# Kernel optimization log

Measured on AMD Instinct MI355X. Metric: run time of the kernel, lower is better.

## Reference

```python
import jax, jax.numpy as jnp
import numpy as np

TEMPERATURE = 0.5
BATCH_SIZE = 4096
EPS = 1e-8  # torch.nn.CosineSimilarity default eps


def setup_inputs() -> dict:
    key = jax.random.key(0)
    k1, k2 = jax.random.split(key)
    z1 = jax.random.normal(k1, (BATCH_SIZE, 256), dtype=jnp.float32)
    z2 = jax.random.normal(k2, (BATCH_SIZE, 256), dtype=jnp.float32)
    return {"z1": z1, "z2": z2}


def reference(z1, z2):
    B = z1.shape[0]
    N = 2 * B
    reps = jnp.concatenate([z1, z2], axis=0)  # [N, D]
    # Cosine similarity (torch clamps each norm to eps before dividing)
    norms = jnp.maximum(jnp.linalg.norm(reps, axis=1, keepdims=True), EPS)
    z = reps / norms
    sim = z @ z.T  # [N, N] cosine similarity matrix

    # positives: diagonals at offsets +B and -B (they are identical by symmetry,
    # but keep the original concat order: [diag(+B), diag(-B)])
    l_pos = jnp.diagonal(sim, offset=B)
    r_pos = jnp.diagonal(sim, offset=-B)
    positives = jnp.concatenate([l_pos, r_pos])  # [N]

    inv_t = 1.0 / TEMPERATURE
    pos_logit = positives * inv_t  # logits[:, 0]

    # negatives are all off-diagonal entries of each row (the positive pair is
    # thus present twice in the logits, faithful to the original). CE with
    # label 0 => loss_i = logsumexp(logits_i) - logits_i[0].
    neg_logits = jnp.where(jnp.eye(N, dtype=bool), -jnp.inf, sim * inv_t)
    lse = jnp.logaddexp(pos_logit, jax.scipy.special.logsumexp(neg_logits, axis=1))
    loss = jnp.sum(lse - pos_logit) / N
    return loss
```

## Files before the change

### kernel.cpp

```cpp
#include <hip/hip_runtime.h>
#include <hip/hip_bf16.h>
#include <cstdint>
#include <cstddef>
#include <math.h>

#define BSZ   4096
#define NROW  8192
#define DIM   256
#define INV_T 2.0f
#define EPS_N 1e-8f

typedef __attribute__((ext_vector_type(8))) short bf16x8;
typedef __attribute__((ext_vector_type(4))) float f32x4;

__device__ __forceinline__ unsigned short f2bf(float x) {
    __hip_bfloat16 h = __float2bfloat16(x);
    return __builtin_bit_cast(unsigned short, h);
}

__device__ __forceinline__ void load_lds16(const void* g, void* l) {
    __builtin_amdgcn_global_load_lds(
        (const __attribute__((address_space(1))) void*)g,
        (__attribute__((address_space(3))) void*)l,
        16, 0, 0);
}

__global__ __launch_bounds__(256)
void nt_normalize(const float* __restrict__ z1,
                  const float* __restrict__ z2,
                  char* __restrict__ zn2,
                  float* __restrict__ rowsum) {
    const int wave = threadIdx.x >> 6;
    const int lane = threadIdx.x & 63;
    const int row  = blockIdx.x * 4 + wave;
    const float* src = (row < BSZ) ? (z1 + (size_t)row * DIM)
                                   : (z2 + (size_t)(row - BSZ) * DIM);
    const float4 v = ((const float4*)src)[lane];
    float ss = v.x * v.x + v.y * v.y + v.z * v.z + v.w * v.w;
    #pragma unroll
    for (int off = 32; off; off >>= 1) ss += __shfl_xor(ss, off);
    const float rinv = 1.0f / fmaxf(sqrtf(ss), EPS_N);
    ushort4 o;
    o.x = f2bf(v.x * rinv);
    o.y = f2bf(v.y * rinv);
    o.z = f2bf(v.z * rinv);
    o.w = f2bf(v.w * rinv);
    const int s    = row >> 7;
    const int lrow = row & 127;
    const int kc   = lane >> 4;
    const int unit = (lane >> 1) & 7;
    const int half = lane & 1;
    const int u    = unit ^ (lrow & 7);
    *(ushort4*)(zn2 + (size_t)s * 65536 + kc * 16384 + lrow * 128 + u * 16 + half * 8) = o;
    if (lane == 0) rowsum[row] = 0.0f;
}

__global__ __launch_bounds__(256)
void nt_gram(const char* __restrict__ zn2,
             float* __restrict__ rowsum,
             float* __restrict__ pos) {
    const int l = blockIdx.x;
    int bi = (int)((129.0 - sqrt(16641.0 - 8.0 * (double)l)) * 0.5);
    while (64 * (bi + 1) - (bi + 1) * bi / 2 <= l) ++bi;
    while (64 * bi - bi * (bi - 1) / 2 > l) --bi;
    const int bj = bi + (l - (64 * bi - bi * (bi - 1) / 2));

    __shared__ char As[16384];
    __shared__ char Bs[16384];

    const int t    = threadIdx.x;
    const int lane = t & 63;
    const int wave = t >> 6;
    const int wrow = (wave >> 1) * 64;
    const int wcol = (wave & 1) * 64;
    const int q    = lane >> 4;
    const int r16  = lane & 15;
    const int sw   = r16 & 7;

    const char* A2 = zn2 + (size_t)bi * 65536;
    const char* B2 = zn2 + (size_t)bj * 65536;

    f32x4 acc[4][4] = {};

    for (int kc = 0; kc < 4; ++kc) {
        #pragma unroll
        for (int p = 0; p < 4; ++p)
            load_lds16(A2 + kc * 16384 + p * 4096 + t * 16, As + p * 4096 + t * 16);
        #pragma unroll
        for (int p = 0; p < 4; ++p)
            load_lds16(B2 + kc * 16384 + p * 4096 + t * 16, Bs + p * 4096 + t * 16);
        __syncthreads();

        #pragma unroll
        for (int kk = 0; kk < 64; kk += 32) {
            const int cc   = (kk >> 3) + q;
            const int cpos = (cc ^ sw) << 4;
            bf16x8 af[4], bfr[4];
            #pragma unroll
            for (int mi = 0; mi < 4; ++mi)
                af[mi] = *(const bf16x8*)(As + (wrow + mi * 16 + r16) * 128 + cpos);
            #pragma unroll
            for (int ni = 0; ni < 4; ++ni)
                bfr[ni] = *(const bf16x8*)(Bs + (wcol + ni * 16 + r16) * 128 + cpos);
            #pragma unroll
            for (int mi = 0; mi < 4; ++mi)
                #pragma unroll
                for (int ni = 0; ni < 4; ++ni)
                    acc[mi][ni] = __builtin_amdgcn_mfma_f32_16x16x32_bf16(
                        af[mi], bfr[ni], acc[mi][ni], 0, 0, 0);
        }
        __syncthreads();
    }

    const int c = r16;
    const bool diag_block = (bi == bj);
    float colp[4] = {0.f, 0.f, 0.f, 0.f};

    #pragma unroll
    for (int mi = 0; mi < 4; ++mi) {
        #pragma unroll
        for (int r = 0; r < 4; ++r) {
            const int grow = bi * 128 + wrow + mi * 16 + q * 4 + r;
            float s = 0.f;
            #pragma unroll
            for (int ni = 0; ni < 4; ++ni) {
                const int gcol = bj * 128 + wcol + ni * 16 + c;
                const float val = acc[mi][ni][r];
                float e = __expf(val * INV_T);
                e = (grow == gcol) ? 0.f : e;
                s += e;
                colp[ni] += e;
                if (gcol == grow + BSZ) {
                    pos[grow] = val;
                    pos[gcol] = val;
                }
            }
            s += __shfl_xor(s, 1);
            s += __shfl_xor(s, 2);
            s += __shfl_xor(s, 4);
            s += __shfl_xor(s, 8);
            if (c == 0) atomicAdd(&rowsum[grow], s);
        }
    }
    if (!diag_block) {
        #pragma unroll
        for (int ni = 0; ni < 4; ++ni) {
            float cs = colp[ni];
            cs += __shfl_xor(cs, 16);
            cs += __shfl_xor(cs, 32);
            if (q == 0) atomicAdd(&rowsum[bj * 128 + wcol + ni * 16 + c], cs);
        }
    }
}

__global__ __launch_bounds__(1024)
void nt_finalize(const float* __restrict__ rowsum,
                 const float* __restrict__ pos,
                 float* __restrict__ out) {
    float v = 0.f;
    for (int i = threadIdx.x; i < NROW; i += 1024) {
        const float pl = pos[i] * INV_T;
        v += logf(__expf(pl) + rowsum[i]) - pl;
    }
    #pragma unroll
    for (int off = 32; off; off >>= 1) v += __shfl_xor(v, off);
    __shared__ float red[16];
    if ((threadIdx.x & 63) == 0) red[threadIdx.x >> 6] = v;
    __syncthreads();
    if (threadIdx.x == 0) {
        float s = 0.f;
        #pragma unroll
        for (int w = 0; w < 16; ++w) s += red[w];
        out[0] = s * (1.0f / NROW);
    }
}

extern "C" void kernel_launch(void* const* d_in, const int* in_sizes, int n_in,
                              void* d_out, int out_size, void* d_ws, size_t ws_size,
                              hipStream_t stream) {
    const float* z1 = (const float*)d_in[0];
    const float* z2 = (const float*)d_in[1];
    float* out = (float*)d_out;

    char*  zn2    = (char*)d_ws;
    float* rowsum = (float*)((char*)d_ws + (size_t)NROW * DIM * 2);
    float* pos    = rowsum + NROW;

    nt_normalize<<<NROW / 4, 256, 0, stream>>>(z1, z2, zn2, rowsum);
    nt_gram<<<2080, 256, 0, stream>>>(zn2, rowsum, pos);
    nt_finalize<<<1, 1024, 0, stream>>>(rowsum, pos, out);
}
```

Measured before the change: 107.2 us.

## Enlarge gram tiles to 256x256 with double-buffered LDS pipeline and LDS row reductions

Switches the symmetric Gram kernel from 128x128 tiles with 256 threads to 256x256 tiles with 1024 threads, rearranging the normalized bf16 layout to match. K chunks are double-buffered in a 128KB LDS buffer, so global-to-LDS loads overlap MFMA work, using explicit vmcnt waits, barriers and setprio. Row and column exp-sums are reduced in LDS before issuing one global atomic per row, which cuts global atomic traffic. Tiles are remapped in a strided order across blocks. The cost is fewer blocks (528), heavy LDS use that allows one block per CU, and more redundant work on diagonal tiles.

```diff
diff --git a/kernel.cpp b/kernel.cpp
--- a/kernel.cpp
+++ b/kernel.cpp
@@ -9,6 +9,7 @@
 #define DIM   256
 #define INV_T 2.0f
 #define EPS_N 1e-8f
+#define NTILE 528
 
 typedef __attribute__((ext_vector_type(8))) short bf16x8;
 typedef __attribute__((ext_vector_type(4))) float f32x4;
@@ -45,74 +46,103 @@
     o.y = f2bf(v.y * rinv);
     o.z = f2bf(v.z * rinv);
     o.w = f2bf(v.w * rinv);
-    const int s    = row >> 7;
-    const int lrow = row & 127;
+    const int s    = row >> 8;
+    const int lrow = row & 255;
     const int kc   = lane >> 4;
     const int unit = (lane >> 1) & 7;
     const int half = lane & 1;
     const int u    = unit ^ (lrow & 7);
-    *(ushort4*)(zn2 + (size_t)s * 65536 + kc * 16384 + lrow * 128 + u * 16 + half * 8) = o;
+    *(ushort4*)(zn2 + (size_t)s * 131072 + kc * 32768 + lrow * 128 + u * 16 + half * 8) = o;
     if (lane == 0) rowsum[row] = 0.0f;
 }
 
-__global__ __launch_bounds__(256)
+__global__ __launch_bounds__(1024)
 void nt_gram(const char* __restrict__ zn2,
              float* __restrict__ rowsum,
              float* __restrict__ pos) {
-    const int l = blockIdx.x;
-    int bi = (int)((129.0 - sqrt(16641.0 - 8.0 * (double)l)) * 0.5);
-    while (64 * (bi + 1) - (bi + 1) * bi / 2 <= l) ++bi;
-    while (64 * bi - bi * (bi - 1) / 2 > l) --bi;
-    const int bj = bi + (l - (64 * bi - bi * (bi - 1) / 2));
-
-    __shared__ char As[16384];
-    __shared__ char Bs[16384];
+    __shared__ char  ldsbuf[131072];
+    __shared__ float red[512];
+
+    const int bid = blockIdx.x;
+    const int l = (bid & 7) * 66 + (bid >> 3);
+    int bi = (int)((65.0 - sqrt(4225.0 - 8.0 * (double)l)) * 0.5);
+    while (32 * (bi + 1) - (bi + 1) * bi / 2 <= l) ++bi;
+    while (32 * bi - bi * (bi - 1) / 2 > l) --bi;
+    const int bj = bi + (l - (32 * bi - bi * (bi - 1) / 2));
 
     const int t    = threadIdx.x;
     const int lane = t & 63;
     const int wave = t >> 6;
-    const int wrow = (wave >> 1) * 64;
-    const int wcol = (wave & 1) * 64;
+    const int wrow = (wave >> 2) * 64;
+    const int wcol = (wave & 3) * 64;
     const int q    = lane >> 4;
     const int r16  = lane & 15;
     const int sw   = r16 & 7;
-
-    const char* A2 = zn2 + (size_t)bi * 65536;
-    const char* B2 = zn2 + (size_t)bj * 65536;
+    const int t16  = t * 16;
+
+    const char* Asrc = zn2 + (size_t)bi * 131072;
+    const char* Bsrc = zn2 + (size_t)bj * 131072;
 
     f32x4 acc[4][4] = {};
 
-    for (int kc = 0; kc < 4; ++kc) {
-        #pragma unroll
-        for (int p = 0; p < 4; ++p)
-            load_lds16(A2 + kc * 16384 + p * 4096 + t * 16, As + p * 4096 + t * 16);
-        #pragma unroll
-        for (int p = 0; p < 4; ++p)
-            load_lds16(B2 + kc * 16384 + p * 4096 + t * 16, Bs + p * 4096 + t * 16);
-        __syncthreads();
-
-        #pragma unroll
-        for (int kk = 0; kk < 64; kk += 32) {
-            const int cc   = (kk >> 3) + q;
-            const int cpos = (cc ^ sw) << 4;
-            bf16x8 af[4], bfr[4];
-            #pragma unroll
-            for (int mi = 0; mi < 4; ++mi)
-                af[mi] = *(const bf16x8*)(As + (wrow + mi * 16 + r16) * 128 + cpos);
-            #pragma unroll
-            for (int ni = 0; ni < 4; ++ni)
-                bfr[ni] = *(const bf16x8*)(Bs + (wcol + ni * 16 + r16) * 128 + cpos);
-            #pragma unroll
-            for (int mi = 0; mi < 4; ++mi)
-                #pragma unroll
-                for (int ni = 0; ni < 4; ++ni)
-                    acc[mi][ni] = __builtin_amdgcn_mfma_f32_16x16x32_bf16(
-                        af[mi], bfr[ni], acc[mi][ni], 0, 0, 0);
-        }
-        __syncthreads();
-    }
-
-    const int c = r16;
+#define STAGE(kc, dbuf)                                                      \
+    {                                                                        \
+        const char* as_ = Asrc + (kc) * 32768;                               \
+        const char* bs_ = Bsrc + (kc) * 32768;                               \
+        char* ad_ = ldsbuf + (dbuf) * 65536;                                 \
+        char* bd_ = ad_ + 32768;                                             \
+        load_lds16(as_ + t16,         ad_ + t16);                            \
+        load_lds16(as_ + 16384 + t16, ad_ + 16384 + t16);                    \
+        load_lds16(bs_ + t16,         bd_ + t16);                            \
+        load_lds16(bs_ + 16384 + t16, bd_ + 16384 + t16);                    \
+    }
+
+#define KHALF(As_, Bs_, kk)                                                  \
+    {                                                                        \
+        const int cpos = ((((kk) >> 3) + q) ^ sw) << 4;                      \
+        bf16x8 af[4], bfv[4];                                                \
+        _Pragma("unroll")                                                    \
+        for (int mi = 0; mi < 4; ++mi)                                       \
+            af[mi] = *(const bf16x8*)((As_) + (wrow + mi * 16 + r16) * 128 + cpos); \
+        _Pragma("unroll")                                                    \
+        for (int ni = 0; ni < 4; ++ni)                                       \
+            bfv[ni] = *(const bf16x8*)((Bs_) + (wcol + ni * 16 + r16) * 128 + cpos); \
+        __builtin_amdgcn_s_setprio(1);                                       \
+        _Pragma("unroll")                                                    \
+        for (int mi = 0; mi < 4; ++mi)                                       \
+            _Pragma("unroll")                                                \
+            for (int ni = 0; ni < 4; ++ni)                                   \
+                acc[mi][ni] = __builtin_amdgcn_mfma_f32_16x16x32_bf16(       \
+                    af[mi], bfv[ni], acc[mi][ni], 0, 0, 0);                  \
+        __builtin_amdgcn_s_setprio(0);                                       \
+    }
+
+#define K_STEP(nwait, dbuf, do_stage, kc_stage)                              \
+    {                                                                        \
+        asm volatile("s_waitcnt vmcnt(" #nwait ")" ::: "memory");            \
+        __builtin_amdgcn_s_barrier();                                        \
+        const char* As_ = ldsbuf + (dbuf) * 65536;                           \
+        const char* Bs_ = As_ + 32768;                                       \
+        KHALF(As_, Bs_, 0)                                                   \
+        KHALF(As_, Bs_, 32)                                                  \
+        __builtin_amdgcn_s_barrier();                                        \
+        __builtin_amdgcn_sched_barrier(0);                                   \
+        if (do_stage) STAGE(kc_stage, dbuf)                                  \
+    }
+
+    STAGE(0, 0)
+    STAGE(1, 1)
+    K_STEP(4, 0, 1, 2)
+    K_STEP(4, 1, 1, 3)
+    K_STEP(4, 0, 0, 0)
+    K_STEP(0, 1, 0, 0)
+
+    if (t < 512) red[t] = 0.0f;
+    __syncthreads();
+    float* rowacc = red;
+    float* colacc = red + 256;
+
+    const int  c          = r16;
     const bool diag_block = (bi == bj);
     float colp[4] = {0.f, 0.f, 0.f, 0.f};
 
@@ -120,11 +150,12 @@
     for (int mi = 0; mi < 4; ++mi) {
         #pragma unroll
         for (int r = 0; r < 4; ++r) {
-            const int grow = bi * 128 + wrow + mi * 16 + q * 4 + r;
+            const int trow = wrow + mi * 16 + q * 4 + r;
+            const int grow = bi * 256 + trow;
             float s = 0.f;
             #pragma unroll
             for (int ni = 0; ni < 4; ++ni) {
-                const int gcol = bj * 128 + wcol + ni * 16 + c;
+                const int gcol = bj * 256 + wcol + ni * 16 + c;
                 const float val = acc[mi][ni][r];
                 float e = __expf(val * INV_T);
                 e = (grow == gcol) ? 0.f : e;
@@ -139,7 +170,7 @@
             s += __shfl_xor(s, 2);
             s += __shfl_xor(s, 4);
             s += __shfl_xor(s, 8);
-            if (c == 0) atomicAdd(&rowsum[grow], s);
+            if (c == 0) atomicAdd(&rowacc[trow], s);
         }
     }
     if (!diag_block) {
@@ -148,9 +179,18 @@
             float cs = colp[ni];
             cs += __shfl_xor(cs, 16);
             cs += __shfl_xor(cs, 32);
-            if (q == 0) atomicAdd(&rowsum[bj * 128 + wcol + ni * 16 + c], cs);
+            if (q == 0) atomicAdd(&colacc[wcol + ni * 16 + c], cs);
         }
     }
+    __syncthreads();
+    if (t < 256) {
+        atomicAdd(&rowsum[bi * 256 + t], rowacc[t]);
+    } else if (t < 512 && !diag_block) {
+        atomicAdd(&rowsum[bj * 256 + (t - 256)], colacc[t - 256]);
+    }
+#undef STAGE
+#undef KHALF
+#undef K_STEP
 }
 
 __global__ __launch_bounds__(1024)
@@ -164,13 +204,13 @@
     }
     #pragma unroll
     for (int off = 32; off; off >>= 1) v += __shfl_xor(v, off);
-    __shared__ float red[16];
-    if ((threadIdx.x & 63) == 0) red[threadIdx.x >> 6] = v;
+    __shared__ float redf[16];
+    if ((threadIdx.x & 63) == 0) redf[threadIdx.x >> 6] = v;
     __syncthreads();
     if (threadIdx.x == 0) {
         float s = 0.f;
         #pragma unroll
-        for (int w = 0; w < 16; ++w) s += red[w];
+        for (int w = 0; w < 16; ++w) s += redf[w];
         out[0] = s * (1.0f / NROW);
     }
 }
@@ -187,6 +227,6 @@
     float* pos    = rowsum + NROW;
 
     nt_normalize<<<NROW / 4, 256, 0, stream>>>(z1, z2, zn2, rowsum);
-    nt_gram<<<2080, 256, 0, stream>>>(zn2, rowsum, pos);
+    nt_gram<<<NTILE, 1024, 0, stream>>>(zn2, rowsum, pos);
     nt_finalize<<<1, 1024, 0, stream>>>(rowsum, pos, out);
 }
```

After: 105.9 us. Within noise of the previous version (-1.2%).

## Make gram kernel persistent with resident A panel and double-buffered B pipeline

Applied to the files above, without the earlier changes.

Replaces the one-block-per-tile launch of 2080 blocks with 256 persistent 512-thread blocks. Each block walks a contiguous run of upper-triangular tiles, keeping the 128-row A panel resident in LDS (64KB) and double-buffering B k-chunks with manual vmcnt waits, so the next loads overlap the current MFMA work. It also raises MFMA priority around the inner products and interleaves chunk assignment across blocks. The intent is to remove per-tile launch and load-stall overhead and reuse A across tiles. The cost is a larger LDS footprint that lowers occupancy, plus possible load imbalance from uneven tile counts per block.

```diff
diff --git a/kernel.cpp b/kernel.cpp
--- a/kernel.cpp
+++ b/kernel.cpp
@@ -24,6 +24,8 @@
         (__attribute__((address_space(3))) void*)l,
         16, 0, 0);
 }
+
+#define VMWAIT(N) asm volatile("s_waitcnt vmcnt(" #N ")" ::: "memory")
 
 __global__ __launch_bounds__(256)
 void nt_normalize(const float* __restrict__ z1,
@@ -55,101 +57,146 @@
     if (lane == 0) rowsum[row] = 0.0f;
 }
 
-__global__ __launch_bounds__(256)
+__global__ __launch_bounds__(512, 2)
 void nt_gram(const char* __restrict__ zn2,
              float* __restrict__ rowsum,
              float* __restrict__ pos) {
-    const int l = blockIdx.x;
-    int bi = (int)((129.0 - sqrt(16641.0 - 8.0 * (double)l)) * 0.5);
-    while (64 * (bi + 1) - (bi + 1) * bi / 2 <= l) ++bi;
-    while (64 * bi - bi * (bi - 1) / 2 > l) --bi;
-    const int bj = bi + (l - (64 * bi - bi * (bi - 1) / 2));
-
-    __shared__ char As[16384];
-    __shared__ char Bs[16384];
+    __shared__ char Ab[65536];
+    __shared__ char Bb[2][16384];
+
+    const int blk   = blockIdx.x;
+    const int chunk = (blk & 7) * 32 + (blk >> 3);
+    const int lo    = (65 * chunk) >> 3;
+    const int hi    = (65 * (chunk + 1)) >> 3;
+    const int W     = (hi - lo) << 2;
+
+    int bi0 = (int)((129.0 - sqrt(16641.0 - 8.0 * (double)lo)) * 0.5);
+    while (64 * (bi0 + 1) - (bi0 + 1) * bi0 / 2 <= lo) ++bi0;
+    while (64 * bi0 - bi0 * (bi0 - 1) / 2 > lo) --bi0;
+    const int bj0 = bi0 + (lo - (64 * bi0 - bi0 * (bi0 - 1) / 2));
 
     const int t    = threadIdx.x;
     const int lane = t & 63;
     const int wave = t >> 6;
-    const int wrow = (wave >> 1) * 64;
-    const int wcol = (wave & 1) * 64;
+    const int wrow = (wave >> 2) * 64;
+    const int wcol = (wave & 3) * 32;
     const int q    = lane >> 4;
     const int r16  = lane & 15;
     const int sw   = r16 & 7;
-
-    const char* A2 = zn2 + (size_t)bi * 65536;
-    const char* B2 = zn2 + (size_t)bj * 65536;
-
-    f32x4 acc[4][4] = {};
-
-    for (int kc = 0; kc < 4; ++kc) {
-        #pragma unroll
-        for (int p = 0; p < 4; ++p)
-            load_lds16(A2 + kc * 16384 + p * 4096 + t * 16, As + p * 4096 + t * 16);
-        #pragma unroll
-        for (int p = 0; p < 4; ++p)
-            load_lds16(B2 + kc * 16384 + p * 4096 + t * 16, Bs + p * 4096 + t * 16);
-        __syncthreads();
-
+    const int t16  = t * 16;
+
+    auto STAGE_A = [&](int bi) {
+        const char* src = zn2 + (size_t)bi * 65536;
+        #pragma unroll
+        for (int j = 0; j < 8; ++j)
+            load_lds16(src + j * 8192 + t16, Ab + j * 8192 + t16);
+    };
+    auto STAGE_B = [&](int bj, int kc, int slot) {
+        const char* src = zn2 + (size_t)bj * 65536 + kc * 16384;
+        load_lds16(src + t16, Bb[slot] + t16);
+        load_lds16(src + 8192 + t16, Bb[slot] + 8192 + t16);
+    };
+
+    f32x4 acc[4][2] = {};
+
+    auto COMPUTE = [&](int kc, int slot) {
+        const char* As = Ab + kc * 16384;
+        const char* Bs = Bb[slot];
         #pragma unroll
         for (int kk = 0; kk < 64; kk += 32) {
-            const int cc   = (kk >> 3) + q;
-            const int cpos = (cc ^ sw) << 4;
-            bf16x8 af[4], bfr[4];
+            const int cpos = (((kk >> 3) + q) ^ sw) << 4;
+            bf16x8 af[4], bfv[2];
             #pragma unroll
             for (int mi = 0; mi < 4; ++mi)
                 af[mi] = *(const bf16x8*)(As + (wrow + mi * 16 + r16) * 128 + cpos);
             #pragma unroll
-            for (int ni = 0; ni < 4; ++ni)
-                bfr[ni] = *(const bf16x8*)(Bs + (wcol + ni * 16 + r16) * 128 + cpos);
+            for (int ni = 0; ni < 2; ++ni)
+                bfv[ni] = *(const bf16x8*)(Bs + (wcol + ni * 16 + r16) * 128 + cpos);
+            __builtin_amdgcn_s_setprio(1);
             #pragma unroll
             for (int mi = 0; mi < 4; ++mi)
                 #pragma unroll
-                for (int ni = 0; ni < 4; ++ni)
+                for (int ni = 0; ni < 2; ++ni)
                     acc[mi][ni] = __builtin_amdgcn_mfma_f32_16x16x32_bf16(
-                        af[mi], bfr[ni], acc[mi][ni], 0, 0, 0);
-        }
-        __syncthreads();
-    }
-
-    const int c = r16;
-    const bool diag_block = (bi == bj);
-    float colp[4] = {0.f, 0.f, 0.f, 0.f};
-
-    #pragma unroll
-    for (int mi = 0; mi < 4; ++mi) {
-        #pragma unroll
-        for (int r = 0; r < 4; ++r) {
-            const int grow = bi * 128 + wrow + mi * 16 + q * 4 + r;
-            float s = 0.f;
-            #pragma unroll
-            for (int ni = 0; ni < 4; ++ni) {
-                const int gcol = bj * 128 + wcol + ni * 16 + c;
-                const float val = acc[mi][ni][r];
-                float e = __expf(val * INV_T);
-                e = (grow == gcol) ? 0.f : e;
-                s += e;
-                colp[ni] += e;
-                if (gcol == grow + BSZ) {
-                    pos[grow] = val;
-                    pos[gcol] = val;
+                        af[mi], bfv[ni], acc[mi][ni], 0, 0, 0);
+            __builtin_amdgcn_s_setprio(0);
+        }
+    };
+
+    int bi_c = bi0, bj_c = bj0;
+    int bi_s = bi0, bj_s = bj0;
+    bool pend_A = false;
+
+    auto EPILOGUE = [&]() {
+        const bool diag = (bi_c == bj_c);
+        float colp[2] = {0.f, 0.f};
+        #pragma unroll
+        for (int mi = 0; mi < 4; ++mi) {
+            #pragma unroll
+            for (int r = 0; r < 4; ++r) {
+                const int grow = bi_c * 128 + wrow + mi * 16 + q * 4 + r;
+                float s = 0.f;
+                #pragma unroll
+                for (int ni = 0; ni < 2; ++ni) {
+                    const int gcol = bj_c * 128 + wcol + ni * 16 + r16;
+                    const float val = acc[mi][ni][r];
+                    float e = __expf(val * INV_T);
+                    e = (grow == gcol) ? 0.f : e;
+                    s += e;
+                    colp[ni] += e;
+                    if (gcol == grow + BSZ) {
+                        pos[grow] = val;
+                        pos[gcol] = val;
+                    }
                 }
+                s += __shfl_xor(s, 1);
+                s += __shfl_xor(s, 2);
+                s += __shfl_xor(s, 4);
+                s += __shfl_xor(s, 8);
+                if (r16 == 0) atomicAdd(&rowsum[grow], s);
             }
-            s += __shfl_xor(s, 1);
-            s += __shfl_xor(s, 2);
-            s += __shfl_xor(s, 4);
-            s += __shfl_xor(s, 8);
-            if (c == 0) atomicAdd(&rowsum[grow], s);
-        }
-    }
-    if (!diag_block) {
-        #pragma unroll
-        for (int ni = 0; ni < 4; ++ni) {
-            float cs = colp[ni];
-            cs += __shfl_xor(cs, 16);
-            cs += __shfl_xor(cs, 32);
-            if (q == 0) atomicAdd(&rowsum[bj * 128 + wcol + ni * 16 + c], cs);
-        }
+        }
+        if (!diag) {
+            #pragma unroll
+            for (int ni = 0; ni < 2; ++ni) {
+                float cs = colp[ni];
+                cs += __shfl_xor(cs, 16);
+                cs += __shfl_xor(cs, 32);
+                if (q == 0) atomicAdd(&rowsum[bj_c * 128 + wcol + ni * 16 + r16], cs);
+            }
+        }
+        #pragma unroll
+        for (int mi = 0; mi < 4; ++mi)
+            #pragma unroll
+            for (int ni = 0; ni < 2; ++ni)
+                acc[mi][ni] = (f32x4){0.f, 0.f, 0.f, 0.f};
+    };
+
+    STAGE_A(bi0);
+    STAGE_B(bj0, 0, 0);
+    STAGE_B(bj0, 1, 1);
+    VMWAIT(2);
+    __builtin_amdgcn_s_barrier();
+
+    for (int w = 0; w < W; ++w) {
+        const int kc = w & 3;
+        COMPUTE(kc, w & 1);
+        __builtin_amdgcn_s_barrier();
+        if (pend_A) { STAGE_A(bi_s); pend_A = false; }
+        const int  w2   = w + 2;
+        const bool more = (w2 < W);
+        if (more) {
+            if ((w2 & 3) == 0) {
+                if (++bj_s > 63) { ++bi_s; bj_s = bi_s; pend_A = true; }
+            }
+            STAGE_B(bj_s, w2 & 3, w2 & 1);
+        }
+        if (more) { VMWAIT(2); } else { VMWAIT(0); }
+        if (kc == 3) {
+            EPILOGUE();
+            if (++bj_c > 63) { ++bi_c; bj_c = bi_c; }
+        }
+        __builtin_amdgcn_s_barrier();
     }
 }
 
@@ -164,13 +211,13 @@
     }
     #pragma unroll
     for (int off = 32; off; off >>= 1) v += __shfl_xor(v, off);
-    __shared__ float red[16];
-    if ((threadIdx.x & 63) == 0) red[threadIdx.x >> 6] = v;
+    __shared__ float redf[16];
+    if ((threadIdx.x & 63) == 0) redf[threadIdx.x >> 6] = v;
     __syncthreads();
     if (threadIdx.x == 0) {
         float s = 0.f;
         #pragma unroll
-        for (int w = 0; w < 16; ++w) s += red[w];
+        for (int w = 0; w < 16; ++w) s += redf[w];
         out[0] = s * (1.0f / NROW);
     }
 }
@@ -187,6 +234,6 @@
     float* pos    = rowsum + NROW;
 
     nt_normalize<<<NROW / 4, 256, 0, stream>>>(z1, z2, zn2, rowsum);
-    nt_gram<<<2080, 256, 0, stream>>>(zn2, rowsum, pos);
+    nt_gram<<<256, 512, 0, stream>>>(zn2, rowsum, pos);
     nt_finalize<<<1, 1024, 0, stream>>>(rowsum, pos, out);
 }
```

Measured after the change: 123.3 us. 1.15x slower.

## Use 8 waves per gram block with 64x32 warp tiles and vectorize finalize

Applied to the files above, without the earlier changes.

The gram kernel now launches 512 threads (8 waves) per 128x128 tile, with each wave computing a 64x32 sub-tile instead of 64x64. This halves accumulator registers per wave and doubles the waves available to hide LDS and global-load latency. The tile loads are split across more threads, two per operand per thread. The finalize kernel reads rowsum and pos as float4, a minor change. The trade-off is more B-fragment reloads relative to MFMA work per wave, and more atomics and shuffles overall.

```diff
diff --git a/kernel.cpp b/kernel.cpp
--- a/kernel.cpp
+++ b/kernel.cpp
@@ -55,7 +55,7 @@
     if (lane == 0) rowsum[row] = 0.0f;
 }
 
-__global__ __launch_bounds__(256)
+__global__ __launch_bounds__(512, 8)
 void nt_gram(const char* __restrict__ zn2,
              float* __restrict__ rowsum,
              float* __restrict__ pos) {
@@ -71,50 +71,47 @@
     const int t    = threadIdx.x;
     const int lane = t & 63;
     const int wave = t >> 6;
-    const int wrow = (wave >> 1) * 64;
-    const int wcol = (wave & 1) * 64;
+    const int wrow = (wave >> 2) * 64;
+    const int wcol = (wave & 3) * 32;
     const int q    = lane >> 4;
     const int r16  = lane & 15;
     const int sw   = r16 & 7;
+    const int t16  = t * 16;
 
     const char* A2 = zn2 + (size_t)bi * 65536;
     const char* B2 = zn2 + (size_t)bj * 65536;
 
-    f32x4 acc[4][4] = {};
+    f32x4 acc[4][2] = {};
 
     for (int kc = 0; kc < 4; ++kc) {
-        #pragma unroll
-        for (int p = 0; p < 4; ++p)
-            load_lds16(A2 + kc * 16384 + p * 4096 + t * 16, As + p * 4096 + t * 16);
-        #pragma unroll
-        for (int p = 0; p < 4; ++p)
-            load_lds16(B2 + kc * 16384 + p * 4096 + t * 16, Bs + p * 4096 + t * 16);
+        load_lds16(A2 + kc * 16384 + t16,        As + t16);
+        load_lds16(A2 + kc * 16384 + 8192 + t16, As + 8192 + t16);
+        load_lds16(B2 + kc * 16384 + t16,        Bs + t16);
+        load_lds16(B2 + kc * 16384 + 8192 + t16, Bs + 8192 + t16);
         __syncthreads();
 
         #pragma unroll
         for (int kk = 0; kk < 64; kk += 32) {
-            const int cc   = (kk >> 3) + q;
-            const int cpos = (cc ^ sw) << 4;
-            bf16x8 af[4], bfr[4];
+            const int cpos = (((kk >> 3) + q) ^ sw) << 4;
+            bf16x8 af[4], bfv[2];
             #pragma unroll
             for (int mi = 0; mi < 4; ++mi)
                 af[mi] = *(const bf16x8*)(As + (wrow + mi * 16 + r16) * 128 + cpos);
             #pragma unroll
-            for (int ni = 0; ni < 4; ++ni)
-                bfr[ni] = *(const bf16x8*)(Bs + (wcol + ni * 16 + r16) * 128 + cpos);
+            for (int ni = 0; ni < 2; ++ni)
+                bfv[ni] = *(const bf16x8*)(Bs + (wcol + ni * 16 + r16) * 128 + cpos);
             #pragma unroll
             for (int mi = 0; mi < 4; ++mi)
                 #pragma unroll
-                for (int ni = 0; ni < 4; ++ni)
+                for (int ni = 0; ni < 2; ++ni)
                     acc[mi][ni] = __builtin_amdgcn_mfma_f32_16x16x32_bf16(
-                        af[mi], bfr[ni], acc[mi][ni], 0, 0, 0);
+                        af[mi], bfv[ni], acc[mi][ni], 0, 0, 0);
         }
         __syncthreads();
     }
 
-    const int c = r16;
     const bool diag_block = (bi == bj);
-    float colp[4] = {0.f, 0.f, 0.f, 0.f};
+    float colp[2] = {0.f, 0.f};
 
     #pragma unroll
     for (int mi = 0; mi < 4; ++mi) {
@@ -123,8 +120,8 @@
             const int grow = bi * 128 + wrow + mi * 16 + q * 4 + r;
             float s = 0.f;
             #pragma unroll
-            for (int ni = 0; ni < 4; ++ni) {
-                const int gcol = bj * 128 + wcol + ni * 16 + c;
+            for (int ni = 0; ni < 2; ++ni) {
+                const int gcol = bj * 128 + wcol + ni * 16 + r16;
                 const float val = acc[mi][ni][r];
                 float e = __expf(val * INV_T);
                 e = (grow == gcol) ? 0.f : e;
@@ -139,16 +136,16 @@
             s += __shfl_xor(s, 2);
             s += __shfl_xor(s, 4);
             s += __shfl_xor(s, 8);
-            if (c == 0) atomicAdd(&rowsum[grow], s);
+            if (r16 == 0) atomicAdd(&rowsum[grow], s);
         }
     }
     if (!diag_block) {
         #pragma unroll
-        for (int ni = 0; ni < 4; ++ni) {
+        for (int ni = 0; ni < 2; ++ni) {
             float cs = colp[ni];
             cs += __shfl_xor(cs, 16);
             cs += __shfl_xor(cs, 32);
-            if (q == 0) atomicAdd(&rowsum[bj * 128 + wcol + ni * 16 + c], cs);
+            if (q == 0) atomicAdd(&rowsum[bj * 128 + wcol + ni * 16 + r16], cs);
         }
     }
 }
@@ -157,20 +154,28 @@
 void nt_finalize(const float* __restrict__ rowsum,
                  const float* __restrict__ pos,
                  float* __restrict__ out) {
+    const float4* rs4 = (const float4*)rowsum;
+    const float4* ps4 = (const float4*)pos;
     float v = 0.f;
-    for (int i = threadIdx.x; i < NROW; i += 1024) {
-        const float pl = pos[i] * INV_T;
-        v += logf(__expf(pl) + rowsum[i]) - pl;
+    #pragma unroll
+    for (int it = 0; it < 2; ++it) {
+        const int i = it * 1024 + threadIdx.x;
+        const float4 r = rs4[i];
+        const float4 p = ps4[i];
+        v += logf(__expf(p.x * INV_T) + r.x) - p.x * INV_T;
+        v += logf(__expf(p.y * INV_T) + r.y) - p.y * INV_T;
+        v += logf(__expf(p.z * INV_T) + r.z) - p.z * INV_T;
+        v += logf(__expf(p.w * INV_T) + r.w) - p.w * INV_T;
     }
     #pragma unroll
     for (int off = 32; off; off >>= 1) v += __shfl_xor(v, off);
-    __shared__ float red[16];
-    if ((threadIdx.x & 63) == 0) red[threadIdx.x >> 6] = v;
+    __shared__ float redf[16];
+    if ((threadIdx.x & 63) == 0) redf[threadIdx.x >> 6] = v;
     __syncthreads();
     if (threadIdx.x == 0) {
         float s = 0.f;
         #pragma unroll
-        for (int w = 0; w < 16; ++w) s += red[w];
+        for (int w = 0; w < 16; ++w) s += redf[w];
         out[0] = s * (1.0f / NROW);
     }
 }
@@ -187,6 +192,6 @@
     float* pos    = rowsum + NROW;
 
     nt_normalize<<<NROW / 4, 256, 0, stream>>>(z1, z2, zn2, rowsum);
-    nt_gram<<<2080, 256, 0, stream>>>(zn2, rowsum, pos);
+    nt_gram<<<2080, 512, 0, stream>>>(zn2, rowsum, pos);
     nt_finalize<<<1, 1024, 0, stream>>>(rowsum, pos, out);
 }
```

Result: slower. 134.0 us (+24.9%).
